# Kernel optimization log

Measured on AMD Instinct MI355X. Metric: run time of the kernel, lower is better.

The kernel has to match this reference:

```python
import jax, jax.numpy as jnp
import numpy as np

N = 50000      # nodes (patients)
E = 500000     # directed edges
H = 128        # Config.HIDDEN_DIM
GH = 256       # Config.GRAPH_HIDDEN
C = 14         # Config.NUM_CLASSES


def setup_inputs() -> dict:
    key = jax.random.key(0)
    ks = jax.random.split(key, 24)
    s = 0.02
    inp = {
        "h_v": jax.random.normal(ks[0], (N, H), jnp.float32),
        "h_t": jax.random.normal(ks[1], (N, H), jnp.float32),
        "h_tab": jax.random.normal(ks[2], (N, H), jnp.float32),
        "edge_index": jax.random.randint(ks[3], (2, E), 0, N, jnp.int64),
        # SAGEConv1: in=3H, out=GH  (lin_l on mean-aggr neighbors w/ bias, lin_r on root, no bias)
        "W1l": jax.random.normal(ks[4], (3 * H, GH), jnp.float32) * s,
        "W1r": jax.random.normal(ks[5], (3 * H, GH), jnp.float32) * s,
        "b1g": jnp.zeros((GH,), jnp.float32),
        # SAGEConv2: in=GH, out=H
        "W2l": jax.random.normal(ks[6], (GH, H), jnp.float32) * s,
        "W2r": jax.random.normal(ks[7], (GH, H), jnp.float32) * s,
        "b2g": jnp.zeros((H,), jnp.float32),
        # projections H->H
        "Wsh": jax.random.normal(ks[8], (H, H), jnp.float32) * s,
        "bsh": jnp.zeros((H,), jnp.float32),
        "Wst": jax.random.normal(ks[9], (H, H), jnp.float32) * s,
        "bst": jnp.zeros((H,), jnp.float32),
        "Wstab": jax.random.normal(ks[10], (H, H), jnp.float32) * s,
        "bstab": jnp.zeros((H,), jnp.float32),
        # classifier 4H -> 256 -> C
        "Wc1": jax.random.normal(ks[11], (4 * H, 256), jnp.float32) * s,
        "bc1": jnp.zeros((256,), jnp.float32),
        "Wc2": jax.random.normal(ks[12], (256, C), jnp.float32) * s,
        "bc2": jnp.zeros((C,), jnp.float32),
    }
    return inp


def _sage_conv(x, src, dst, Wl, Wr, b):
    # PyG SAGEConv with mean aggregation (eval mode):
    # out = mean_{j in N(i)} x_j @ Wl + b  +  x_i @ Wr
    n = x.shape[0]
    agg = jax.ops.segment_sum(x[src], dst, num_segments=n)          # [N, d_in]
    cnt = jax.ops.segment_sum(jnp.ones((src.shape[0],), x.dtype), dst, num_segments=n)
    mean = agg / jnp.maximum(cnt, 1.0)[:, None]
    return mean @ Wl + b + x @ Wr


def reference(h_v, h_t, h_tab, edge_index,
              W1l, W1r, b1g, W2l, W2r, b2g,
              Wsh, bsh, Wst, bst, Wstab, bstab,
              Wc1, bc1, Wc2, bc2):
    src, dst = edge_index[0], edge_index[1]
    node_feats = jnp.concatenate([h_v, h_t, h_tab], axis=1)          # [N, 3H]
    h_g = jax.nn.relu(_sage_conv(node_feats, src, dst, W1l, W1r, b1g))
    h_g = _sage_conv(h_g, src, dst, W2l, W2r, b2g)                   # [N, H]
    # F.normalize(p=2, dim=1)
    h_g = h_g / jnp.maximum(jnp.linalg.norm(h_g, axis=1, keepdims=True), 1e-12)
    z_shared = h_g @ Wsh + bsh
    z_t = h_t @ Wst + bst
    z_tab = h_tab @ Wstab + bstab
    combined = jnp.concatenate([z_shared, z_t, z_tab, h_g], axis=1)  # [N, 4H]
    logits = jax.nn.relu(combined @ Wc1 + bc1) @ Wc2 + bc2           # [N, C]
    return (logits, z_shared, z_t, z_tab)
```

## Files before the change

kernel.cpp:

```cpp
#include <hip/hip_runtime.h>
#include <math.h>

typedef __attribute__((ext_vector_type(8))) short short8;
typedef __attribute__((ext_vector_type(4))) float f32x4;
typedef __attribute__((ext_vector_type(4))) unsigned int u32x4;

static __device__ __forceinline__ unsigned short f2bf(float f) {
    union { float f; unsigned int u; } v; v.f = f;
    unsigned int r = v.u + 0x7fffu + ((v.u >> 16) & 1u);
    return (unsigned short)(r >> 16);
}
static __device__ __forceinline__ float bflo(unsigned int u) {
    union { unsigned int u; float f; } v; v.u = u << 16; return v.f;
}
static __device__ __forceinline__ float bfhi(unsigned int u) {
    union { unsigned int u; float f; } v; v.u = u & 0xffff0000u; return v.f;
}

typedef __attribute__((address_space(1))) const unsigned int gu32;
typedef __attribute__((address_space(3))) unsigned int lu32;
static __device__ __forceinline__ void gload16(const void* g, void* l) {
    __builtin_amdgcn_global_load_lds((gu32*)g, (lu32*)l, 16, 0, 0);
}

__global__ void zero_buf(u32x4* __restrict__ a, int n16)
{
    int i = blockIdx.x * blockDim.x + threadIdx.x;
    if (i < n16) a[i] = (u32x4){0u, 0u, 0u, 0u};
}

__global__ void convert_x(const float* __restrict__ hv, const float* __restrict__ ht,
                          const float* __restrict__ htab, unsigned short* __restrict__ X,
                          int total )
{
    int idx = blockIdx.x * blockDim.x + threadIdx.x;
    if (idx >= total) return;
    int r = idx / 96;
    int c4 = idx - r * 96;
    int seg = c4 >> 5;
    const float* s = (seg == 0) ? hv : (seg == 1) ? ht : htab;
    float4 v = ((const float4*)s)[(size_t)r * 32 + (c4 & 31)];
    ushort4 o;
    o.x = f2bf(v.x); o.y = f2bf(v.y); o.z = f2bf(v.z); o.w = f2bf(v.w);
    *(ushort4*)(X + (size_t)r * 384 + c4 * 4) = o;
}

struct WDesc { const float* src; int K; int N; int dstoff; };
struct WPack { WDesc w[9]; };
__global__ void convert_w(WPack p, unsigned short* __restrict__ dst)
{
    WDesc d = p.w[blockIdx.y];
    int total = d.K * d.N;
    for (int i = blockIdx.x * blockDim.x + threadIdx.x; i < total;
         i += gridDim.x * blockDim.x) {
        int k = i / d.N, n = i - k * d.N;
        dst[d.dstoff + (size_t)n * d.K + k] = f2bf(d.src[i]);
    }
}

struct GemmP {
    const unsigned short* A; int lda;
    const unsigned short* Bt;
    const float* bias;
    float* Cf; int ldcf;
    unsigned short* Cb; int ldcb;
};
struct GemmP3 { GemmP q[3]; };

template<int MODE, int NP>
__global__ __launch_bounds__(256, 4) void gemm4(GemmP3 ps, int M, int K)
{
    __shared__ __align__(16) unsigned short smem[128 * 64 * 2];
    unsigned short* As = smem;
    unsigned short* Bs = smem + 128 * 64;
    const GemmP P = ps.q[(MODE == 1) ? blockIdx.z : 0];
    const int tid = threadIdx.x;
    const int lane = tid & 63;
    const int wid = tid >> 6;
    const int wr = wid >> 1, wc = wid & 1;
    const int bid = blockIdx.x;
    const int q = bid >> 3;
    const int m0 = ((bid & 7) + 8 * (q / NP)) * 128;
    const int n0 = (q % NP) * 128;

    const int lrow = lane >> 3;
    const int lchk = (lane & 7) ^ lrow;
    const unsigned short* gA[4];
    #pragma unroll
    for (int i = 0; i < 4; ++i) {
        int r = m0 + wid * 32 + i * 8 + lrow;
        if (r > M - 1) r = M - 1;
        gA[i] = P.A + (size_t)r * P.lda + lchk * 8;
    }
    const unsigned short* gB[4];
    #pragma unroll
    for (int i = 0; i < 4; ++i) {
        int r = n0 + wid * 32 + i * 8 + lrow;
        gB[i] = P.Bt + (size_t)r * K + lchk * 8;
    }
    unsigned short* lA = As + wid * 32 * 64;
    unsigned short* lB = Bs + wid * 32 * 64;

    f32x4 acc[4][4] = {};
    const int nt = K >> 6;
    for (int t = 0; t < nt; ++t) {
        __syncthreads();
        #pragma unroll
        for (int i = 0; i < 4; ++i) gload16(gA[i] + t * 64, lA + i * 8 * 64);
        #pragma unroll
        for (int i = 0; i < 4; ++i) gload16(gB[i] + t * 64, lB + i * 8 * 64);
        asm volatile("s_waitcnt vmcnt(0)" ::: "memory");
        __syncthreads();
        #pragma unroll
        for (int kk = 0; kk < 2; ++kk) {
            int g = kk * 4 + (lane >> 4);
            short8 a[4], b[4];
            #pragma unroll
            for (int mi = 0; mi < 4; ++mi) {
                int row = wr * 64 + mi * 16 + (lane & 15);
                a[mi] = *(const short8*)(As + row * 64 + ((g ^ (row & 7)) * 8));
            }
            #pragma unroll
            for (int ni = 0; ni < 4; ++ni) {
                int row = wc * 64 + ni * 16 + (lane & 15);
                b[ni] = *(const short8*)(Bs + row * 64 + ((g ^ (row & 7)) * 8));
            }
            #pragma unroll
            for (int mi = 0; mi < 4; ++mi)
                #pragma unroll
                for (int ni = 0; ni < 4; ++ni)
                    acc[mi][ni] = __builtin_amdgcn_mfma_f32_16x16x32_bf16(
                        a[mi], b[ni], acc[mi][ni], 0, 0, 0);
        }
    }

    if (MODE == 0) {
        unsigned short* stage = smem;
        #pragma unroll
        for (int half = 0; half < 2; ++half) {
            __syncthreads();
            if (wr == half) {
                #pragma unroll
                for (int mi = 0; mi < 4; ++mi)
                    #pragma unroll
                    for (int ni = 0; ni < 4; ++ni) {
                        int colL = wc * 64 + ni * 16 + (lane & 15);
                        #pragma unroll
                        for (int j = 0; j < 4; ++j) {
                            int rel = mi * 16 + ((lane >> 4) << 2) + j;
                            stage[rel * 128 + colL] = f2bf(acc[mi][ni][j]);
                        }
                    }
            }
            __syncthreads();
            #pragma unroll
            for (int p = 0; p < 4; ++p) {
                int idx = p * 256 + tid;
                int r = idx >> 4, c8 = idx & 15;
                int grow = m0 + half * 64 + r;
                if (grow < M)
                    *(u32x4*)(P.Cb + (size_t)grow * P.ldcb + n0 + c8 * 8) =
                        *(const u32x4*)(stage + r * 128 + c8 * 8);
            }
        }
    }

    if (MODE == 1) {
        __syncthreads();
        #pragma unroll
        for (int mi = 0; mi < 4; ++mi)
            #pragma unroll
            for (int ni = 0; ni < 4; ++ni) {
                int colL = wc * 64 + ni * 16 + (lane & 15);
                float bv = P.bias[colL];
                #pragma unroll
                for (int j = 0; j < 4; ++j) {
                    int rL = wr * 64 + mi * 16 + ((lane >> 4) << 2) + j;
                    smem[rL * 128 + colL] = f2bf(acc[mi][ni][j] + bv);
                }
            }
        __syncthreads();
        #pragma unroll
        for (int p = 0; p < 8; ++p) {
            int idx = p * 256 + tid;
            int r = idx >> 4, c8 = idx & 15;
            int grow = m0 + r;
            if (grow < M)
                *(u32x4*)(P.Cb + (size_t)grow * P.ldcb + n0 + c8 * 8) =
                    *(const u32x4*)(smem + r * 128 + c8 * 8);
        }
        float* stagef = (float*)smem;
        #pragma unroll
        for (int half = 0; half < 2; ++half) {
            __syncthreads();
            if (wr == half) {
                #pragma unroll
                for (int mi = 0; mi < 4; ++mi)
                    #pragma unroll
                    for (int ni = 0; ni < 4; ++ni) {
                        int colL = wc * 64 + ni * 16 + (lane & 15);
                        float bv = P.bias[colL];
                        #pragma unroll
                        for (int j = 0; j < 4; ++j) {
                            int rel = mi * 16 + ((lane >> 4) << 2) + j;
                            stagef[rel * 128 + colL] = acc[mi][ni][j] + bv;
                        }
                    }
            }
            __syncthreads();
            #pragma unroll
            for (int p = 0; p < 8; ++p) {
                int idx = p * 256 + tid;
                int r = idx >> 5, c4 = idx & 31;
                int grow = m0 + half * 64 + r;
                if (grow < M)
                    __builtin_nontemporal_store(
                        *(const f32x4*)(stagef + r * 128 + c4 * 4),
                        (f32x4*)(P.Cf + (size_t)grow * P.ldcf + n0 + c4 * 4));
            }
        }
    }
}

__global__ __launch_bounds__(512, 2) void gemm5(
    const unsigned short* __restrict__ A,
    const unsigned short* __restrict__ Bt,
    const float* __restrict__ bias,
    const unsigned short* __restrict__ Wc2t,
    const float* __restrict__ bc2,
    float* __restrict__ logits,
    int M, int K)
{
    __shared__ __align__(16) unsigned short smem[128 * 256];
    unsigned short* As = smem;
    unsigned short* Bs = smem + 128 * 64;
    const int tid = threadIdx.x;
    const int lane = tid & 63;
    const int wid = tid >> 6;
    const int wr = wid >> 2;
    const int wc = wid & 3;
    const int m0 = blockIdx.x * 128;

    const int lrow = lane >> 3;
    const int lchk = (lane & 7) ^ lrow;
    const unsigned short* gA[2];
    #pragma unroll
    for (int i = 0; i < 2; ++i) {
        int r = m0 + wid * 16 + i * 8 + lrow;
        if (r > M - 1) r = M - 1;
        gA[i] = A + (size_t)r * K + lchk * 8;
    }
    const unsigned short* gB[4];
    #pragma unroll
    for (int i = 0; i < 4; ++i) {
        int r = wid * 32 + i * 8 + lrow;
        gB[i] = Bt + (size_t)r * K + lchk * 8;
    }
    unsigned short* lA = As + wid * 16 * 64;
    unsigned short* lB = Bs + wid * 32 * 64;

    f32x4 acc[4][4] = {};
    const int nt = K >> 6;
    for (int t = 0; t < nt; ++t) {
        __syncthreads();
        #pragma unroll
        for (int i = 0; i < 2; ++i) gload16(gA[i] + t * 64, lA + i * 8 * 64);
        #pragma unroll
        for (int i = 0; i < 4; ++i) gload16(gB[i] + t * 64, lB + i * 8 * 64);
        asm volatile("s_waitcnt vmcnt(0)" ::: "memory");
        __syncthreads();
        #pragma unroll
        for (int kk = 0; kk < 2; ++kk) {
            int g = kk * 4 + (lane >> 4);
            short8 a[4], b[4];
            #pragma unroll
            for (int mi = 0; mi < 4; ++mi) {
                int row = wr * 64 + mi * 16 + (lane & 15);
                a[mi] = *(const short8*)(As + row * 64 + ((g ^ (row & 7)) * 8));
            }
            #pragma unroll
            for (int ni = 0; ni < 4; ++ni) {
                int row = wc * 64 + ni * 16 + (lane & 15);
                b[ni] = *(const short8*)(Bs + row * 64 + ((g ^ (row & 7)) * 8));
            }
            #pragma unroll
            for (int mi = 0; mi < 4; ++mi)
                #pragma unroll
                for (int ni = 0; ni < 4; ++ni)
                    acc[mi][ni] = __builtin_amdgcn_mfma_f32_16x16x32_bf16(
                        a[mi], b[ni], acc[mi][ni], 0, 0, 0);
        }
    }

    __syncthreads();
    #pragma unroll
    for (int mi = 0; mi < 4; ++mi)
        #pragma unroll
        for (int ni = 0; ni < 4; ++ni) {
            int colL = wc * 64 + ni * 16 + (lane & 15);
            float bv = bias[colL];
            #pragma unroll
            for (int j = 0; j < 4; ++j) {
                int rL = wr * 64 + mi * 16 + ((lane >> 4) << 2) + j;
                float x = fmaxf(acc[mi][ni][j] + bv, 0.0f);
                int c8 = colL >> 3;
                smem[rL * 256 + ((c8 ^ (rL & 7)) * 8) + (colL & 7)] = f2bf(x);
            }
        }
    __syncthreads();
    f32x4 lacc = {0.f, 0.f, 0.f, 0.f};
    int rL = wid * 16 + (lane & 15);
    #pragma unroll
    for (int k0 = 0; k0 < 256; k0 += 32) {
        int c8 = (k0 >> 3) + (lane >> 4);
        short8 a = *(const short8*)(smem + rL * 256 + ((c8 ^ (rL & 7)) * 8));
        short8 b = *(const short8*)(Wc2t + (lane & 15) * 256 + k0 + (lane >> 4) * 8);
        lacc = __builtin_amdgcn_mfma_f32_16x16x32_bf16(a, b, lacc, 0, 0, 0);
    }
    int colL = lane & 15;
    if (colL < 14) {
        float bb = bc2[colL];
        #pragma unroll
        for (int j = 0; j < 4; ++j) {
            int r = m0 + wid * 16 + (lane >> 4) * 4 + j;
            if (r < M)
                __builtin_nontemporal_store(lacc[j] + bb,
                    logits + (size_t)r * 14 + colL);
        }
    }
}

__global__ void count_deg(const int* __restrict__ dst, int* __restrict__ deg, int E)
{
    int e = blockIdx.x * blockDim.x + threadIdx.x;
    if (e < E) atomicAdd(&deg[dst[e]], 1);
}

__global__ __launch_bounds__(1024) void scan_part(
    const int* __restrict__ deg, int* __restrict__ off, int* __restrict__ sums, int N)
{
    __shared__ int buf[1024];
    int i = blockIdx.x * 1024 + threadIdx.x;
    int v = (i < N) ? deg[i] : 0;
    buf[threadIdx.x] = v;
    __syncthreads();
    #pragma unroll
    for (int o = 1; o < 1024; o <<= 1) {
        int t = (threadIdx.x >= o) ? buf[threadIdx.x - o] : 0;
        __syncthreads();
        buf[threadIdx.x] += t;
        __syncthreads();
    }
    if (i < N) off[i] = buf[threadIdx.x] - v;
    if (threadIdx.x == 1023) sums[blockIdx.x] = buf[1023];
}

__global__ void scan_sums(int* __restrict__ sums, int* __restrict__ offN, int nb)
{
    int lane = threadIdx.x;
    int v = (lane < nb) ? sums[lane] : 0;
    int incl = v;
    #pragma unroll
    for (int o = 1; o < 64; o <<= 1) {
        int t = __shfl_up(incl, o);
        if (lane >= o) incl += t;
    }
    if (lane < nb) sums[lane] = incl - v;
    if (lane == 63) *offN = incl;
}

__global__ __launch_bounds__(1024) void scan_add(
    const int* __restrict__ sums, int* __restrict__ off,
    int* __restrict__ cursor, int N)
{
    int i = blockIdx.x * 1024 + threadIdx.x;
    if (i < N) {
        int v = off[i] + sums[blockIdx.x];
        off[i] = v;
        cursor[i] = v;
    }
}

__global__ void fill_csr(const int* __restrict__ src, const int* __restrict__ dst,
                         int* __restrict__ cursor, int* __restrict__ csr, int E)
{
    int e = blockIdx.x * blockDim.x + threadIdx.x;
    if (e < E) {
        int p = atomicAdd(&cursor[dst[e]], 1);
        csr[p] = src[e];
    }
}

__global__ __launch_bounds__(256) void sage1_gather(
    const unsigned short* __restrict__ y1,
    const int* __restrict__ off, const int* __restrict__ csr,
    const float* __restrict__ b, unsigned short* __restrict__ out, int N)
{
    int lane = threadIdx.x & 63;
    int node = blockIdx.x * 4 + (threadIdx.x >> 6);
    if (node >= N) return;
    int s = off[node], e = off[node + 1];
    int half = lane >> 5, l32 = lane & 31;
    float a[8] = {};
    int p = s + half;
    for (; p + 6 < e; p += 8) {
        int j0 = csr[p],     j1 = csr[p + 2];
        int j2 = csr[p + 4], j3 = csr[p + 6];
        uint4 v0 = *(const uint4*)(y1 + (size_t)j0 * 512 + l32 * 8);
        uint4 v1 = *(const uint4*)(y1 + (size_t)j1 * 512 + l32 * 8);
        uint4 v2 = *(const uint4*)(y1 + (size_t)j2 * 512 + l32 * 8);
        uint4 v3 = *(const uint4*)(y1 + (size_t)j3 * 512 + l32 * 8);
        a[0] += bflo(v0.x); a[1] += bfhi(v0.x); a[2] += bflo(v0.y); a[3] += bfhi(v0.y);
        a[4] += bflo(v0.z); a[5] += bfhi(v0.z); a[6] += bflo(v0.w); a[7] += bfhi(v0.w);
        a[0] += bflo(v1.x); a[1] += bfhi(v1.x); a[2] += bflo(v1.y); a[3] += bfhi(v1.y);
        a[4] += bflo(v1.z); a[5] += bfhi(v1.z); a[6] += bflo(v1.w); a[7] += bfhi(v1.w);
        a[0] += bflo(v2.x); a[1] += bfhi(v2.x); a[2] += bflo(v2.y); a[3] += bfhi(v2.y);
        a[4] += bflo(v2.z); a[5] += bfhi(v2.z); a[6] += bflo(v2.w); a[7] += bfhi(v2.w);
        a[0] += bflo(v3.x); a[1] += bfhi(v3.x); a[2] += bflo(v3.y); a[3] += bfhi(v3.y);
        a[4] += bflo(v3.z); a[5] += bfhi(v3.z); a[6] += bflo(v3.w); a[7] += bfhi(v3.w);
    }
    for (; p + 2 < e; p += 4) {
        int j0 = csr[p], j1 = csr[p + 2];
        uint4 v0 = *(const uint4*)(y1 + (size_t)j0 * 512 + l32 * 8);
        uint4 v1 = *(const uint4*)(y1 + (size_t)j1 * 512 + l32 * 8);
        a[0] += bflo(v0.x); a[1] += bfhi(v0.x); a[2] += bflo(v0.y); a[3] += bfhi(v0.y);
        a[4] += bflo(v0.z); a[5] += bfhi(v0.z); a[6] += bflo(v0.w); a[7] += bfhi(v0.w);
        a[0] += bflo(v1.x); a[1] += bfhi(v1.x); a[2] += bflo(v1.y); a[3] += bfhi(v1.y);
        a[4] += bflo(v1.z); a[5] += bfhi(v1.z); a[6] += bflo(v1.w); a[7] += bfhi(v1.w);
    }
    for (; p < e; p += 2) {
        int j = csr[p];
        uint4 v = *(const uint4*)(y1 + (size_t)j * 512 + l32 * 8);
        a[0] += bflo(v.x); a[1] += bfhi(v.x); a[2] += bflo(v.y); a[3] += bfhi(v.y);
        a[4] += bflo(v.z); a[5] += bfhi(v.z); a[6] += bflo(v.w); a[7] += bfhi(v.w);
    }
    #pragma unroll
    for (int i = 0; i < 8; ++i) a[i] += __shfl_xor(a[i], 32);
    if (half == 0) {
        float inv = (e > s) ? 1.0f / (float)(e - s) : 1.0f;
        uint4 rv = *(const uint4*)(y1 + (size_t)node * 512 + 256 + l32 * 8);
        float4 b0 = ((const float4*)b)[l32 * 2];
        float4 b1 = ((const float4*)b)[l32 * 2 + 1];
        float r[8] = {bflo(rv.x), bfhi(rv.x), bflo(rv.y), bfhi(rv.y),
                      bflo(rv.z), bfhi(rv.z), bflo(rv.w), bfhi(rv.w)};
        float bb[8] = {b0.x, b0.y, b0.z, b0.w, b1.x, b1.y, b1.z, b1.w};
        u32x4 vv;
        #pragma unroll
        for (int i = 0; i < 4; ++i) {
            unsigned int lo = f2bf(fmaxf(a[2*i]   * inv + bb[2*i]   + r[2*i],   0.f));
            unsigned int hi = f2bf(fmaxf(a[2*i+1] * inv + bb[2*i+1] + r[2*i+1], 0.f));
            vv[i] = lo | (hi << 16);
        }
        *(u32x4*)(out + (size_t)node * 256 + l32 * 8) = vv;
    }
}

__global__ __launch_bounds__(256) void sage2_gather_norm(
    const unsigned short* __restrict__ y2,
    const int* __restrict__ off, const int* __restrict__ csr,
    const float* __restrict__ b, unsigned short* __restrict__ outb, int N)
{
    int lane = threadIdx.x & 63;
    int node = blockIdx.x * 4 + (threadIdx.x >> 6);
    if (node >= N) return;
    int s = off[node], e = off[node + 1];
    int grp = lane >> 4, l16 = lane & 15;
    float a[8] = {};
    int p = s + grp;
    for (; p + 4 < e; p += 8) {
        int j0 = csr[p], j1 = csr[p + 4];
        uint4 v0 = *(const uint4*)(y2 + (size_t)j0 * 256 + l16 * 8);
        uint4 v1 = *(const uint4*)(y2 + (size_t)j1 * 256 + l16 * 8);
        a[0] += bflo(v0.x); a[1] += bfhi(v0.x); a[2] += bflo(v0.y); a[3] += bfhi(v0.y);
        a[4] += bflo(v0.z); a[5] += bfhi(v0.z); a[6] += bflo(v0.w); a[7] += bfhi(v0.w);
        a[0] += bflo(v1.x); a[1] += bfhi(v1.x); a[2] += bflo(v1.y); a[3] += bfhi(v1.y);
        a[4] += bflo(v1.z); a[5] += bfhi(v1.z); a[6] += bflo(v1.w); a[7] += bfhi(v1.w);
    }
    for (; p < e; p += 4) {
        int j = csr[p];
        uint4 v = *(const uint4*)(y2 + (size_t)j * 256 + l16 * 8);
        a[0] += bflo(v.x); a[1] += bfhi(v.x); a[2] += bflo(v.y); a[3] += bfhi(v.y);
        a[4] += bflo(v.z); a[5] += bfhi(v.z); a[6] += bflo(v.w); a[7] += bfhi(v.w);
    }
    #pragma unroll
    for (int i = 0; i < 8; ++i) {
        a[i] += __shfl_xor(a[i], 16);
        a[i] += __shfl_xor(a[i], 32);
    }
    if (grp == 0) {
        float inv = (e > s) ? 1.0f / (float)(e - s) : 1.0f;
        uint4 rv = *(const uint4*)(y2 + (size_t)node * 256 + 128 + l16 * 8);
        float4 b0 = ((const float4*)b)[l16 * 2];
        float4 b1 = ((const float4*)b)[l16 * 2 + 1];
        float r[8] = {bflo(rv.x), bfhi(rv.x), bflo(rv.y), bfhi(rv.y),
                      bflo(rv.z), bfhi(rv.z), bflo(rv.w), bfhi(rv.w)};
        float bb[8] = {b0.x, b0.y, b0.z, b0.w, b1.x, b1.y, b1.z, b1.w};
        float h[8];
        float ss = 0.f;
        #pragma unroll
        for (int i = 0; i < 8; ++i) {
            h[i] = a[i] * inv + bb[i] + r[i];
            ss += h[i] * h[i];
        }
        ss += __shfl_xor(ss, 1);
        ss += __shfl_xor(ss, 2);
        ss += __shfl_xor(ss, 4);
        ss += __shfl_xor(ss, 8);
        float sc = 1.0f / fmaxf(sqrtf(ss), 1e-12f);
        u32x4 vv;
        #pragma unroll
        for (int i = 0; i < 4; ++i) {
            unsigned int lo = f2bf(h[2*i] * sc);
            unsigned int hi = f2bf(h[2*i+1] * sc);
            vv[i] = lo | (hi << 16);
        }
        *(u32x4*)(outb + (size_t)node * 512 + l16 * 8) = vv;
    }
}

extern "C" void kernel_launch(void* const* d_in, const int* in_sizes, int n_in,
                              void* d_out, int out_size, void* d_ws, size_t ws_size,
                              hipStream_t stream)
{
    const float* h_v   = (const float*)d_in[0];
    const float* h_t   = (const float*)d_in[1];
    const float* h_tab = (const float*)d_in[2];
    const int*   eidx  = (const int*)d_in[3];
    const float* W1l = (const float*)d_in[4];
    const float* W1r = (const float*)d_in[5];
    const float* b1g = (const float*)d_in[6];
    const float* W2l = (const float*)d_in[7];
    const float* W2r = (const float*)d_in[8];
    const float* b2g = (const float*)d_in[9];
    const float* Wsh = (const float*)d_in[10];
    const float* bsh = (const float*)d_in[11];
    const float* Wst = (const float*)d_in[12];
    const float* bst = (const float*)d_in[13];
    const float* Wstab = (const float*)d_in[14];
    const float* bstab = (const float*)d_in[15];
    const float* Wc1 = (const float*)d_in[16];
    const float* bc1 = (const float*)d_in[17];
    const float* Wc2 = (const float*)d_in[18];
    const float* bc2 = (const float*)d_in[19];

    const int N = in_sizes[0] / 128;
    const int E = in_sizes[3] / 2;
    const int* src = eidx;
    const int* dst = eidx + E;

    int* deg    = (int*)d_ws;
    int* off    = deg + N;
    int* cursor = off + N + 1;
    int* csr    = cursor + N;
    int* sums   = csr + E;
    size_t int_bytes = ((size_t)3 * N + 1 + E + 64) * 4;
    unsigned short* Wt = (unsigned short*)((char*)d_ws + ((int_bytes + 255) & ~(size_t)255));
    const int oW1l = 0;
    const int oW1r = oW1l + 98304;
    const int oW2l = oW1r + 98304;
    const int oW2r = oW2l + 32768;
    const int oWsh = oW2r + 32768;
    const int oWst = oWsh + 16384;
    const int oWstab = oWst + 16384;
    const int oWc1 = oWstab + 16384;
    const int oWc2t = oWc1 + 131072;
    const int wtotal = oWc2t + 4096;

    unsigned short* Xbf   = Wt + wtotal;
    unsigned short* bufY  = Xbf + (size_t)N * 384;
    unsigned short* bufH  = bufY + (size_t)N * 512;
    unsigned short* bufY2 = bufH + (size_t)N * 256;

    float* out    = (float*)d_out;
    float* logits = out;
    float* z_sh   = out + (size_t)N * 14;
    float* z_t    = z_sh + (size_t)N * 128;
    float* z_tab  = z_t + (size_t)N * 128;

    const int gx = (N + 127) / 128;
    const int gxp = (gx + 7) & ~7;
    const int nb = (N + 1023) / 1024;

    {
        int n16 = (N * 4) / 16;
        zero_buf<<<(n16 + 255) / 256, 256, 0, stream>>>((u32x4*)deg, n16);
        zero_buf<<<2, 256, 0, stream>>>((u32x4*)(Wt + oWc2t), 512);
    }
    count_deg<<<(E + 255) / 256, 256, 0, stream>>>(dst, deg, E);
    scan_part<<<nb, 1024, 0, stream>>>(deg, off, sums, N);
    scan_sums<<<1, 64, 0, stream>>>(sums, off + N, nb);
    scan_add<<<nb, 1024, 0, stream>>>(sums, off, cursor, N);
    fill_csr<<<(E + 255) / 256, 256, 0, stream>>>(src, dst, cursor, csr, E);

    convert_x<<<(N * 96 + 255) / 256, 256, 0, stream>>>(h_v, h_t, h_tab, Xbf, N * 96);
    WPack p;
    p.w[0] = {W1l, 384, 256, oW1l};     p.w[1] = {W1r, 384, 256, oW1r};
    p.w[2] = {W2l, 256, 128, oW2l};     p.w[3] = {W2r, 256, 128, oW2r};
    p.w[4] = {Wsh, 128, 128, oWsh};     p.w[5] = {Wst, 128, 128, oWst};
    p.w[6] = {Wstab, 128, 128, oWstab}; p.w[7] = {Wc1, 512, 256, oWc1};
    p.w[8] = {Wc2, 256, 14, oWc2t};
    convert_w<<<dim3(128, 9), 256, 0, stream>>>(p, Wt);

    unsigned short* y1 = bufY;
    {
        GemmP3 g{};
        g.q[0] = {Xbf, 384, Wt + oW1l, nullptr, nullptr, 0, y1, 512};
        gemm4<0, 4><<<dim3(gxp * 4), 256, 0, stream>>>(g, N, 384);
    }

    sage1_gather<<<(N + 3) / 4, 256, 0, stream>>>(y1, off, csr, b1g, bufH, N);

    {
        GemmP3 g{};
        g.q[0] = {bufH, 256, Wt + oW2l, nullptr, nullptr, 0, bufY2, 256};
        gemm4<0, 2><<<dim3(gxp * 2), 256, 0, stream>>>(g, N, 256);
    }

    unsigned short* cls_bf = bufY;
    sage2_gather_norm<<<(N + 3) / 4, 256, 0, stream>>>(bufY2, off, csr, b2g,
        cls_bf + 384, N);

    {
        GemmP3 g{};
        g.q[0] = {cls_bf + 384, 512, Wt + oWsh,   bsh,   z_sh,  128, cls_bf + 0,   512};
        g.q[1] = {Xbf + 128,    384, Wt + oWst,   bst,   z_t,   128, cls_bf + 128, 512};
        g.q[2] = {Xbf + 256,    384, Wt + oWstab, bstab, z_tab, 128, cls_bf + 256, 512};
        gemm4<1, 1><<<dim3(gxp, 1, 3), 256, 0, stream>>>(g, N, 128);
    }

    gemm5<<<dim3(gxp), 512, 0, stream>>>(cls_bf, Wt + oWc1, bc1,
        Wt + oWc2t, bc2, logits, N, 512);
}
```

Baseline: 251.6 us.

## Use 128x256 tiles with 512-thread blocks for the SAGE feature GEMMs

The two MODE-0 GEMMs (X@[W1l|W1r] and H@[W2l|W2r]) move from a 256-thread 128x128-tile kernel to a new 512-thread kernel with 128x256 output tiles and 8 waves arranged 2x4. This halves the number of blocks and lets each A tile loaded into LDS be reused across twice as many output columns, reducing redundant A traffic. The bias/fp32-output projection path is split into its own non-templated kernel with the same math. The cost is more LDS per block (48 KB), lower block-level occupancy, and fewer blocks to spread across CUs.

```diff
diff --git a/kernel.cpp b/kernel.cpp
--- a/kernel.cpp
+++ b/kernel.cpp
@@ -67,38 +67,42 @@
 };
 struct GemmP3 { GemmP q[3]; };
 
-template<int MODE, int NP>
-__global__ __launch_bounds__(256, 4) void gemm4(GemmP3 ps, int M, int K)
-{
-    __shared__ __align__(16) unsigned short smem[128 * 64 * 2];
+template<int NP>
+__global__ __launch_bounds__(512, 2) void gemm7(
+    const unsigned short* __restrict__ A, int lda,
+    const unsigned short* __restrict__ Bt,
+    unsigned short* __restrict__ Cb, int ldcb,
+    int M, int K)
+{
+    __shared__ __align__(16) unsigned short smem[(128 + 256) * 64];
     unsigned short* As = smem;
     unsigned short* Bs = smem + 128 * 64;
-    const GemmP P = ps.q[(MODE == 1) ? blockIdx.z : 0];
     const int tid = threadIdx.x;
     const int lane = tid & 63;
     const int wid = tid >> 6;
-    const int wr = wid >> 1, wc = wid & 1;
+    const int wr = wid >> 2;
+    const int wc = wid & 3;
     const int bid = blockIdx.x;
     const int q = bid >> 3;
     const int m0 = ((bid & 7) + 8 * (q / NP)) * 128;
-    const int n0 = (q % NP) * 128;
+    const int n0 = (q % NP) * 256;
 
     const int lrow = lane >> 3;
     const int lchk = (lane & 7) ^ lrow;
-    const unsigned short* gA[4];
-    #pragma unroll
-    for (int i = 0; i < 4; ++i) {
-        int r = m0 + wid * 32 + i * 8 + lrow;
+    const unsigned short* gA[2];
+    #pragma unroll
+    for (int i = 0; i < 2; ++i) {
+        int r = m0 + wid * 16 + i * 8 + lrow;
         if (r > M - 1) r = M - 1;
-        gA[i] = P.A + (size_t)r * P.lda + lchk * 8;
+        gA[i] = A + (size_t)r * lda + lchk * 8;
     }
     const unsigned short* gB[4];
     #pragma unroll
     for (int i = 0; i < 4; ++i) {
         int r = n0 + wid * 32 + i * 8 + lrow;
-        gB[i] = P.Bt + (size_t)r * K + lchk * 8;
-    }
-    unsigned short* lA = As + wid * 32 * 64;
+        gB[i] = Bt + (size_t)r * K + lchk * 8;
+    }
+    unsigned short* lA = As + wid * 16 * 64;
     unsigned short* lB = Bs + wid * 32 * 64;
 
     f32x4 acc[4][4] = {};
@@ -106,7 +110,7 @@
     for (int t = 0; t < nt; ++t) {
         __syncthreads();
         #pragma unroll
-        for (int i = 0; i < 4; ++i) gload16(gA[i] + t * 64, lA + i * 8 * 64);
+        for (int i = 0; i < 2; ++i) gload16(gA[i] + t * 64, lA + i * 8 * 64);
         #pragma unroll
         for (int i = 0; i < 4; ++i) gload16(gB[i] + t * 64, lB + i * 8 * 64);
         asm volatile("s_waitcnt vmcnt(0)" ::: "memory");
@@ -134,90 +138,152 @@
         }
     }
 
-    if (MODE == 0) {
-        unsigned short* stage = smem;
-        #pragma unroll
-        for (int half = 0; half < 2; ++half) {
-            __syncthreads();
-            if (wr == half) {
+    unsigned short* stage = smem;
+    #pragma unroll
+    for (int half = 0; half < 2; ++half) {
+        __syncthreads();
+        if (wr == half) {
+            #pragma unroll
+            for (int mi = 0; mi < 4; ++mi)
                 #pragma unroll
-                for (int mi = 0; mi < 4; ++mi)
+                for (int ni = 0; ni < 4; ++ni) {
+                    int colL = wc * 64 + ni * 16 + (lane & 15);
                     #pragma unroll
-                    for (int ni = 0; ni < 4; ++ni) {
-                        int colL = wc * 64 + ni * 16 + (lane & 15);
-                        #pragma unroll
-                        for (int j = 0; j < 4; ++j) {
-                            int rel = mi * 16 + ((lane >> 4) << 2) + j;
-                            stage[rel * 128 + colL] = f2bf(acc[mi][ni][j]);
-                        }
+                    for (int j = 0; j < 4; ++j) {
+                        int rel = mi * 16 + ((lane >> 4) << 2) + j;
+                        stage[rel * 256 + colL] = f2bf(acc[mi][ni][j]);
                     }
-            }
-            __syncthreads();
-            #pragma unroll
-            for (int p = 0; p < 4; ++p) {
-                int idx = p * 256 + tid;
-                int r = idx >> 4, c8 = idx & 15;
-                int grow = m0 + half * 64 + r;
-                if (grow < M)
-                    *(u32x4*)(P.Cb + (size_t)grow * P.ldcb + n0 + c8 * 8) =
-                        *(const u32x4*)(stage + r * 128 + c8 * 8);
-            }
-        }
-    }
-
-    if (MODE == 1) {
-        __syncthreads();
-        #pragma unroll
-        for (int mi = 0; mi < 4; ++mi)
+                }
+        }
+        __syncthreads();
+        #pragma unroll
+        for (int p = 0; p < 4; ++p) {
+            int idx = p * 512 + tid;
+            int r = idx >> 5, c8 = idx & 31;
+            int grow = m0 + half * 64 + r;
+            if (grow < M)
+                *(u32x4*)(Cb + (size_t)grow * ldcb + n0 + c8 * 8) =
+                    *(const u32x4*)(stage + r * 256 + c8 * 8);
+        }
+    }
+}
+
+struct GemmP3x { GemmP q[3]; };
+
+__global__ __launch_bounds__(256, 4) void gemm4p(GemmP3 ps, int M, int K)
+{
+    __shared__ __align__(16) unsigned short smem[128 * 64 * 2];
+    unsigned short* As = smem;
+    unsigned short* Bs = smem + 128 * 64;
+    const GemmP P = ps.q[blockIdx.z];
+    const int tid = threadIdx.x;
+    const int lane = tid & 63;
+    const int wid = tid >> 6;
+    const int wr = wid >> 1, wc = wid & 1;
+    const int m0 = blockIdx.x * 128;
+
+    const int lrow = lane >> 3;
+    const int lchk = (lane & 7) ^ lrow;
+    const unsigned short* gA[4];
+    #pragma unroll
+    for (int i = 0; i < 4; ++i) {
+        int r = m0 + wid * 32 + i * 8 + lrow;
+        if (r > M - 1) r = M - 1;
+        gA[i] = P.A + (size_t)r * P.lda + lchk * 8;
+    }
+    const unsigned short* gB[4];
+    #pragma unroll
+    for (int i = 0; i < 4; ++i) {
+        int r = wid * 32 + i * 8 + lrow;
+        gB[i] = P.Bt + (size_t)r * K + lchk * 8;
+    }
+    unsigned short* lA = As + wid * 32 * 64;
+    unsigned short* lB = Bs + wid * 32 * 64;
+
+    f32x4 acc[4][4] = {};
+    const int nt = K >> 6;
+    for (int t = 0; t < nt; ++t) {
+        __syncthreads();
+        #pragma unroll
+        for (int i = 0; i < 4; ++i) gload16(gA[i] + t * 64, lA + i * 8 * 64);
+        #pragma unroll
+        for (int i = 0; i < 4; ++i) gload16(gB[i] + t * 64, lB + i * 8 * 64);
+        asm volatile("s_waitcnt vmcnt(0)" ::: "memory");
+        __syncthreads();
+        #pragma unroll
+        for (int kk = 0; kk < 2; ++kk) {
+            int g = kk * 4 + (lane >> 4);
+            short8 a[4], b[4];
+            #pragma unroll
+            for (int mi = 0; mi < 4; ++mi) {
+                int row = wr * 64 + mi * 16 + (lane & 15);
+                a[mi] = *(const short8*)(As + row * 64 + ((g ^ (row & 7)) * 8));
+            }
             #pragma unroll
             for (int ni = 0; ni < 4; ++ni) {
-                int colL = wc * 64 + ni * 16 + (lane & 15);
-                float bv = P.bias[colL];
+                int row = wc * 64 + ni * 16 + (lane & 15);
+                b[ni] = *(const short8*)(Bs + row * 64 + ((g ^ (row & 7)) * 8));
+            }
+            #pragma unroll
+            for (int mi = 0; mi < 4; ++mi)
                 #pragma unroll
-                for (int j = 0; j < 4; ++j) {
-                    int rL = wr * 64 + mi * 16 + ((lane >> 4) << 2) + j;
-                    smem[rL * 128 + colL] = f2bf(acc[mi][ni][j] + bv);
+                for (int ni = 0; ni < 4; ++ni)
+                    acc[mi][ni] = __builtin_amdgcn_mfma_f32_16x16x32_bf16(
+                        a[mi], b[ni], acc[mi][ni], 0, 0, 0);
+        }
+    }
+
+    __syncthreads();
+    #pragma unroll
+    for (int mi = 0; mi < 4; ++mi)
+        #pragma unroll
+        for (int ni = 0; ni < 4; ++ni) {
+            int colL = wc * 64 + ni * 16 + (lane & 15);
+            float bv = P.bias[colL];
+            #pragma unroll
+            for (int j = 0; j < 4; ++j) {
+                int rL = wr * 64 + mi * 16 + ((lane >> 4) << 2) + j;
+                smem[rL * 128 + colL] = f2bf(acc[mi][ni][j] + bv);
+            }
+        }
+    __syncthreads();
+    #pragma unroll
+    for (int p = 0; p < 8; ++p) {
+        int idx = p * 256 + tid;
+        int r = idx >> 4, c8 = idx & 15;
+        int grow = m0 + r;
+        if (grow < M)
+            *(u32x4*)(P.Cb + (size_t)grow * P.ldcb + c8 * 8) =
+                *(const u32x4*)(smem + r * 128 + c8 * 8);
+    }
+    float* stagef = (float*)smem;
+    #pragma unroll
+    for (int half = 0; half < 2; ++half) {
+        __syncthreads();
+        if (wr == half) {
+            #pragma unroll
+            for (int mi = 0; mi < 4; ++mi)
+                #pragma unroll
+                for (int ni = 0; ni < 4; ++ni) {
+                    int colL = wc * 64 + ni * 16 + (lane & 15);
+                    float bv = P.bias[colL];
+                    #pragma unroll
+                    for (int j = 0; j < 4; ++j) {
+                        int rel = mi * 16 + ((lane >> 4) << 2) + j;
+                        stagef[rel * 128 + colL] = acc[mi][ni][j] + bv;
+                    }
                 }
-            }
+        }
         __syncthreads();
         #pragma unroll
         for (int p = 0; p < 8; ++p) {
             int idx = p * 256 + tid;
-            int r = idx >> 4, c8 = idx & 15;
-            int grow = m0 + r;
+            int r = idx >> 5, c4 = idx & 31;
+            int grow = m0 + half * 64 + r;
             if (grow < M)
-                *(u32x4*)(P.Cb + (size_t)grow * P.ldcb + n0 + c8 * 8) =
-                    *(const u32x4*)(smem + r * 128 + c8 * 8);
-        }
-        float* stagef = (float*)smem;
-        #pragma unroll
-        for (int half = 0; half < 2; ++half) {
-            __syncthreads();
-            if (wr == half) {
-                #pragma unroll
-                for (int mi = 0; mi < 4; ++mi)
-                    #pragma unroll
-                    for (int ni = 0; ni < 4; ++ni) {
-                        int colL = wc * 64 + ni * 16 + (lane & 15);
-                        float bv = P.bias[colL];
-                        #pragma unroll
-                        for (int j = 0; j < 4; ++j) {
-                            int rel = mi * 16 + ((lane >> 4) << 2) + j;
-                            stagef[rel * 128 + colL] = acc[mi][ni][j] + bv;
-                        }
-                    }
-            }
-            __syncthreads();
-            #pragma unroll
-            for (int p = 0; p < 8; ++p) {
-                int idx = p * 256 + tid;
-                int r = idx >> 5, c4 = idx & 31;
-                int grow = m0 + half * 64 + r;
-                if (grow < M)
-                    __builtin_nontemporal_store(
-                        *(const f32x4*)(stagef + r * 128 + c4 * 4),
-                        (f32x4*)(P.Cf + (size_t)grow * P.ldcf + n0 + c4 * 4));
-            }
+                __builtin_nontemporal_store(
+                    *(const f32x4*)(stagef + r * 128 + c4 * 4),
+                    (f32x4*)(P.Cf + (size_t)grow * P.ldcf + c4 * 4));
         }
     }
 }
@@ -602,19 +668,11 @@
     convert_w<<<dim3(128, 9), 256, 0, stream>>>(p, Wt);
 
     unsigned short* y1 = bufY;
-    {
-        GemmP3 g{};
-        g.q[0] = {Xbf, 384, Wt + oW1l, nullptr, nullptr, 0, y1, 512};
-        gemm4<0, 4><<<dim3(gxp * 4), 256, 0, stream>>>(g, N, 384);
-    }
+    gemm7<2><<<dim3(gxp * 2), 512, 0, stream>>>(Xbf, 384, Wt + oW1l, y1, 512, N, 384);
 
     sage1_gather<<<(N + 3) / 4, 256, 0, stream>>>(y1, off, csr, b1g, bufH, N);
 
-    {
-        GemmP3 g{};
-        g.q[0] = {bufH, 256, Wt + oW2l, nullptr, nullptr, 0, bufY2, 256};
-        gemm4<0, 2><<<dim3(gxp * 2), 256, 0, stream>>>(g, N, 256);
-    }
+    gemm7<1><<<dim3(gxp), 512, 0, stream>>>(bufH, 256, Wt + oW2l, bufY2, 256, N, 256);
 
     unsigned short* cls_bf = bufY;
     sage2_gather_norm<<<(N + 3) / 4, 256, 0, stream>>>(bufY2, off, csr, b2g,
@@ -625,7 +683,7 @@
         g.q[0] = {cls_bf + 384, 512, Wt + oWsh,   bsh,   z_sh,  128, cls_bf + 0,   512};
         g.q[1] = {Xbf + 128,    384, Wt + oWst,   bst,   z_t,   128, cls_bf + 128, 512};
         g.q[2] = {Xbf + 256,    384, Wt + oWstab, bstab, z_tab, 128, cls_bf + 256, 512};
-        gemm4<1, 1><<<dim3(gxp, 1, 3), 256, 0, stream>>>(g, N, 128);
+        gemm4p<<<dim3(gxp, 1, 3), 256, 0, stream>>>(g, N, 128);
     }
 
     gemm5<<<dim3(gxp), 512, 0, stream>>>(cls_bf, Wt + oWc1, bc1,
```

Result: no change. 253.3 us (+0.7%).
